# Kernel tuning notes

Measured on AMD Instinct MI355X. Metric: run time of the kernel, lower is better.

The kernel has to match this reference:

```python
import jax, jax.numpy as jnp
import numpy as np

N, E, W, G = 100000, 625000, 128, 64  # nodes, edges, width, num graphs
EPS = 1e-5


def setup_inputs() -> dict:
    key = jax.random.key(0)
    ks = jax.random.split(key, 8)
    x = jax.random.normal(ks[0], (N, W), jnp.float32)
    edge_index = jax.random.randint(ks[1], (2, E), 0, N, dtype=jnp.int32)
    edge_weight = jax.random.uniform(ks[2], (E,), jnp.float32)
    batch_map = jnp.sort(jax.random.randint(ks[3], (N,), 0, G, dtype=jnp.int32))
    s = 1.0 / np.sqrt(W)
    return {
        "x": x,
        "edge_index": edge_index,
        "edge_weight": edge_weight,
        "batch_map": batch_map,
        "gn_weight": jnp.ones((W,), jnp.float32),
        "gn_bias": jnp.zeros((W,), jnp.float32),
        "gn_mean_scale": jnp.ones((W,), jnp.float32),
        "W_rel1": jax.random.normal(ks[4], (W, W), jnp.float32) * s,
        "b_rel1": jnp.zeros((W,), jnp.float32),
        "W_root1": jax.random.normal(ks[5], (W, W), jnp.float32) * s,
        "W_rel2": jax.random.normal(ks[6], (W, W), jnp.float32) * s,
        "b_rel2": jnp.zeros((W,), jnp.float32),
        "W_root2": jax.random.normal(ks[7], (W, W), jnp.float32) * s,
    }


def _graph_norm(x, batch, weight, bias, mean_scale):
    # per-graph mean / var keyed on batch_map (PyG GraphNorm)
    cnt = jax.ops.segment_sum(jnp.ones((x.shape[0], 1), x.dtype), batch, num_segments=G)
    mean = jax.ops.segment_sum(x, batch, num_segments=G) / cnt
    out = x - mean_scale * mean[batch]
    var = jax.ops.segment_sum(out * out, batch, num_segments=G) / cnt
    std = jnp.sqrt(var + EPS)
    return weight * out / std[batch] + bias


def _graph_conv(x, src, dst, ew, W_rel, b_rel, W_root):
    # out_i = W_rel @ sum_{j->i} e_ji * x_j + b_rel + W_root @ x_i
    msg = x[src] * ew[:, None]                       # [E, W] gather
    agg = jax.ops.segment_sum(msg, dst, num_segments=x.shape[0])  # scatter-add
    return agg @ W_rel.T + b_rel + x @ W_root.T


def reference(x, edge_index, edge_weight, batch_map,
              gn_weight, gn_bias, gn_mean_scale,
              W_rel1, b_rel1, W_root1, W_rel2, b_rel2, W_root2):
    src, dst = edge_index[0], edge_index[1]
    xx = _graph_norm(x, batch_map, gn_weight, gn_bias, gn_mean_scale)
    xx = _graph_conv(xx, src, dst, edge_weight, W_rel1, b_rel1, W_root1)
    xx = jnp.where(xx >= 0, xx, 0.1 * xx)            # LeakyReLU(0.1)
    xx = _graph_conv(xx, src, dst, edge_weight, W_rel2, b_rel2, W_root2)
    return x + xx
```

## Files before the change

kernel.cpp:

```cpp
#include <hip/hip_runtime.h>
#include <hip/hip_bf16.h>

#define WW 128
#define GG 64
#define GN_EPS 1e-5f
#define SCAN_B 1024

typedef __attribute__((ext_vector_type(8))) short short8;
typedef __attribute__((ext_vector_type(4))) float floatx4;

__device__ inline float bf2f(__hip_bfloat16 h) { return __bfloat162float(h); }
__device__ inline float bfbits2f(short v) {
    return __uint_as_float(((unsigned)(unsigned short)v) << 16);
}
__device__ inline short f2bfbits(float f) {
    __hip_bfloat16 h = __float2bfloat16(f);
    return *reinterpret_cast<short*>(&h);
}

__global__ __launch_bounds__(128) void stats_kernel(
    const float* __restrict__ x, const int* __restrict__ batch, int N,
    float* __restrict__ gsum, float* __restrict__ gsumsq, float* __restrict__ gcnt)
{
    int w = threadIdx.x;
    int row0 = blockIdx.x * 64;
    int row1 = min(row0 + 64, N);
    float s = 0.f, ss = 0.f;
    int cur = batch[row0];
    int cnt = 0;
    auto flush = [&]() {
        atomicAdd(&gsum[cur * WW + w], s);
        atomicAdd(&gsumsq[cur * WW + w], ss);
        if (w == 0) atomicAdd(&gcnt[cur], (float)cnt);
        s = 0.f; ss = 0.f; cnt = 0;
    };
    int i = row0;
    for (; i + 4 <= row1; i += 4) {
        int g0 = batch[i + 0], g1 = batch[i + 1], g2 = batch[i + 2], g3 = batch[i + 3];
        float v0 = x[(size_t)(i + 0) * WW + w];
        float v1 = x[(size_t)(i + 1) * WW + w];
        float v2 = x[(size_t)(i + 2) * WW + w];
        float v3 = x[(size_t)(i + 3) * WW + w];
        if (g0 != cur) { flush(); cur = g0; }
        s += v0; ss += v0 * v0; ++cnt;
        if (g1 != cur) { flush(); cur = g1; }
        s += v1; ss += v1 * v1; ++cnt;
        if (g2 != cur) { flush(); cur = g2; }
        s += v2; ss += v2 * v2; ++cnt;
        if (g3 != cur) { flush(); cur = g3; }
        s += v3; ss += v3 * v3; ++cnt;
    }
    for (; i < row1; ++i) {
        int g = batch[i];
        float v = x[(size_t)i * WW + w];
        if (g != cur) { flush(); cur = g; }
        s += v; ss += v * v; ++cnt;
    }
    flush();
}

__global__ __launch_bounds__(256) void finalize_kernel(
    const float* __restrict__ gsum, const float* __restrict__ gsumsq,
    const float* __restrict__ gcnt,
    const float* __restrict__ wgt, const float* __restrict__ bias,
    const float* __restrict__ ms,
    float* __restrict__ scalev, float* __restrict__ shiftv)
{
    int idx = blockIdx.x * blockDim.x + threadIdx.x;
    if (idx >= GG * WW) return;
    int g = idx >> 7, w = idx & (WW - 1);
    float cnt = gcnt[g];
    float inv = cnt > 0.f ? 1.f / cnt : 0.f;
    float mean = gsum[idx] * inv;
    float msw = ms[w];
    float var = gsumsq[idx] * inv - mean * mean * msw * (2.f - msw);
    var = fmaxf(var, 0.f);
    float sc = wgt[w] * rsqrtf(var + GN_EPS);
    scalev[idx] = sc;
    shiftv[idx] = bias[w] - sc * msw * mean;
}

__global__ __launch_bounds__(256) void normalize_kernel(
    const float* __restrict__ x, const int* __restrict__ batch,
    const float* __restrict__ scalev, const float* __restrict__ shiftv,
    __hip_bfloat16* __restrict__ xn, int N)
{
    size_t tid = (size_t)blockIdx.x * blockDim.x + threadIdx.x;
    if (tid >= (size_t)N * (WW / 4)) return;
    int row = (int)(tid >> 5);
    int c4 = (int)(tid & 31) * 4;
    int g = batch[row];
    float4 v = *(const float4*)(x + (size_t)row * WW + c4);
    float4 sc = *(const float4*)(scalev + (size_t)g * WW + c4);
    float4 sh = *(const float4*)(shiftv + (size_t)g * WW + c4);
    __hip_bfloat162 o0, o1;
    o0.x = __float2bfloat16(sc.x * v.x + sh.x);
    o0.y = __float2bfloat16(sc.y * v.y + sh.y);
    o1.x = __float2bfloat16(sc.z * v.z + sh.z);
    o1.y = __float2bfloat16(sc.w * v.w + sh.w);
    union { __hip_bfloat162 h[2]; uint2 u; } pk;
    pk.h[0] = o0; pk.h[1] = o1;
    *(uint2*)(xn + (size_t)row * WW + c4) = pk.u;
}

__global__ __launch_bounds__(256) void cvt_w_kernel(
    const float* __restrict__ w0, const float* __restrict__ w1,
    const float* __restrict__ w2, const float* __restrict__ w3,
    __hip_bfloat16* __restrict__ dst)
{
    int idx = blockIdx.x * blockDim.x + threadIdx.x;
    int m = idx >> 14;
    int o = idx & 16383;
    const float* src = (m == 0) ? w0 : (m == 1) ? w1 : (m == 2) ? w2 : w3;
    dst[idx] = __float2bfloat16(src[o]);
}

__global__ __launch_bounds__(256) void hist_kernel(
    const int* __restrict__ ei, int E, int* __restrict__ deg)
{
    int e = blockIdx.x * 256 + threadIdx.x;
    if (e < E) atomicAdd(&deg[ei[(size_t)E + e]], 1);
}

__global__ __launch_bounds__(SCAN_B) void scan_blocks(
    const int* __restrict__ deg, int N, int* __restrict__ off, int* __restrict__ bsum)
{
    __shared__ int s[SCAN_B];
    int t = threadIdx.x;
    int i = blockIdx.x * SCAN_B + t;
    int v = (i < N) ? deg[i] : 0;
    s[t] = v; __syncthreads();
    for (int d = 1; d < SCAN_B; d <<= 1) {
        int tmp = (t >= d) ? s[t - d] : 0;
        __syncthreads();
        s[t] += tmp;
        __syncthreads();
    }
    if (i < N) off[i] = s[t] - v;
    if (t == SCAN_B - 1) bsum[blockIdx.x] = s[t];
}

__global__ __launch_bounds__(256) void scan_partials(int* __restrict__ bsum, int P)
{
    __shared__ int s[256];
    int t = threadIdx.x;
    int v = (t < P) ? bsum[t] : 0;
    s[t] = v; __syncthreads();
    for (int d = 1; d < 256; d <<= 1) {
        int tmp = (t >= d) ? s[t - d] : 0;
        __syncthreads();
        s[t] += tmp;
        __syncthreads();
    }
    if (t < P) bsum[t] = s[t] - v;
}

__global__ __launch_bounds__(SCAN_B) void add_offsets(
    int* __restrict__ off, const int* __restrict__ bsum, int N)
{
    int i = blockIdx.x * SCAN_B + threadIdx.x;
    if (i < N) off[i] += bsum[blockIdx.x];
}

__global__ __launch_bounds__(256) void place_kernel(
    const int* __restrict__ ei, const float* __restrict__ ew,
    const int* __restrict__ off, int* __restrict__ cursor,
    int2* __restrict__ ebuf, int E)
{
    int base = blockIdx.x * 1024 + threadIdx.x;
    int dstv[4], srcv[4];
    float wv[4];
    int slot[4];
#pragma unroll
    for (int i = 0; i < 4; ++i) {
        int e = base + i * 256;
        dstv[i] = (e < E) ? ei[(size_t)E + e] : -1;
    }
#pragma unroll
    for (int i = 0; i < 4; ++i) {
        int e = base + i * 256;
        if (e < E) { srcv[i] = ei[e]; wv[i] = ew[e]; }
    }
#pragma unroll
    for (int i = 0; i < 4; ++i)
        if (dstv[i] >= 0) slot[i] = off[dstv[i]] + atomicAdd(&cursor[dstv[i]], 1);
#pragma unroll
    for (int i = 0; i < 4; ++i)
        if (dstv[i] >= 0) ebuf[slot[i]] = make_int2(srcv[i], __float_as_int(wv[i]));
}

template <bool OUT_BF16>
__global__ __launch_bounds__(256, 4) void fused_kernel(
    const __hip_bfloat16* __restrict__ X,
    const int2* __restrict__ ebuf, const int* __restrict__ off,
    const int* __restrict__ deg,
    const __hip_bfloat16* __restrict__ Wrel, const __hip_bfloat16* __restrict__ Wroot,
    const float* __restrict__ bias, const float* __restrict__ resid,
    void* __restrict__ outv, int N, int leaky)
{
    __shared__ __hip_bfloat16 smem[2 * 32 * 128];
    int tid = threadIdx.x;
    int wave = tid >> 6, lane = tid & 63;
    int q = lane >> 4, r16 = lane & 15;
    int rb = blockIdx.x * 32;

#pragma unroll
    for (int s = 0; s < 2; ++s) {
        int t = wave * 2 + s;
        int rloc = t * 4 + (lane >> 4);
        int c = (lane & 15) ^ (rloc & 15);
        int grow = rb + rloc; if (grow >= N) grow = N - 1;
        const __hip_bfloat16* g = X + (size_t)grow * WW + c * 8;
        __hip_bfloat16* l = smem + 4096 + t * 512;
        __builtin_amdgcn_global_load_lds(
            (const __attribute__((address_space(1))) void*)g,
            (__attribute__((address_space(3))) void*)l, 16, 0, 0);
    }

    int node = rb + (tid >> 3);
    int nc = node < N ? node : N - 1;
    int start = off[nc];
    int d = (node < N) ? deg[nc] : 0;
    int sub = tid & 7;
    float a16[16];
#pragma unroll
    for (int j = 0; j < 16; ++j) a16[j] = 0.f;
    int last = start + d - 1;
    for (int k = start; k <= last; k += 2) {
        int i1 = min(k + 1, last);
        int2 p0 = ebuf[k];
        int2 p1 = ebuf[i1];
        const __hip_bfloat16* r0 = X + (size_t)p0.x * WW + sub * 16;
        const __hip_bfloat16* r1 = X + (size_t)p1.x * WW + sub * 16;
        short8 a0 = *(const short8*)(r0);
        short8 b0 = *(const short8*)(r0 + 8);
        short8 a1 = *(const short8*)(r1);
        short8 b1 = *(const short8*)(r1 + 8);
        float w0 = __int_as_float(p0.y);
        float w1 = (k + 1 <= last) ? __int_as_float(p1.y) : 0.f;
#pragma unroll
        for (int j = 0; j < 8; ++j) {
            a16[j]     += w0 * bfbits2f(a0[j]) + w1 * bfbits2f(a1[j]);
            a16[8 + j] += w0 * bfbits2f(b0[j]) + w1 * bfbits2f(b1[j]);
        }
    }

    {
        int r = tid >> 3;
        short8 pk0, pk1;
#pragma unroll
        for (int j = 0; j < 8; ++j) {
            pk0[j] = f2bfbits(a16[j]);
            pk1[j] = f2bfbits(a16[8 + j]);
        }
        int s0 = (2 * sub)     ^ (r & 15);
        int s1 = (2 * sub + 1) ^ (r & 15);
        *(short8*)(smem + r * 128 + s0 * 8) = pk0;
        *(short8*)(smem + r * 128 + s1 * 8) = pk1;
    }

    short8 wf[8][2];
#pragma unroll
    for (int kc = 0; kc < 8; ++kc) {
        const __hip_bfloat16* Wsel = (kc < 4) ? Wrel : Wroot;
        int koff = (kc & 3) * 32 + q * 8;
#pragma unroll
        for (int tt = 0; tt < 2; ++tt) {
            int col = wave * 32 + 2 * r16 + tt;
            wf[kc][tt] = *(const short8*)(Wsel + ((size_t)col * WW + koff));
        }
    }
    float bcol[2];
#pragma unroll
    for (int tt = 0; tt < 2; ++tt) bcol[tt] = bias[wave * 32 + 2 * r16 + tt];

    __syncthreads();

    floatx4 acc[2][2];
#pragma unroll
    for (int r = 0; r < 2; ++r)
#pragma unroll
        for (int tt = 0; tt < 2; ++tt) acc[r][tt] = (floatx4){0.f, 0.f, 0.f, 0.f};

#pragma unroll
    for (int kc = 0; kc < 8; ++kc) {
        int m = kc >> 2;
        short8 af[2];
#pragma unroll
        for (int r = 0; r < 2; ++r) {
            int row = r * 16 + r16;
            int slot = ((kc & 3) * 4 + q) ^ r16;
            af[r] = *(const short8*)(&smem[m * 4096 + row * 128 + slot * 8]);
        }
#pragma unroll
        for (int r = 0; r < 2; ++r) {
            acc[r][0] = __builtin_amdgcn_mfma_f32_16x16x32_bf16(af[r], wf[kc][0], acc[r][0], 0, 0, 0);
            acc[r][1] = __builtin_amdgcn_mfma_f32_16x16x32_bf16(af[r], wf[kc][1], acc[r][1], 0, 0, 0);
        }
    }

    int colb = wave * 32 + 2 * r16;
#pragma unroll
    for (int r = 0; r < 2; ++r)
#pragma unroll
        for (int rr = 0; rr < 4; ++rr) {
            int row = rb + r * 16 + q * 4 + rr;
            if (row < N) {
                float v0 = acc[r][0][rr] + bcol[0];
                float v1 = acc[r][1][rr] + bcol[1];
                if (leaky) {
                    v0 = v0 >= 0.f ? v0 : 0.1f * v0;
                    v1 = v1 >= 0.f ? v1 : 0.1f * v1;
                }
                if (OUT_BF16) {
                    __hip_bfloat162 o;
                    o.x = __float2bfloat16(v0);
                    o.y = __float2bfloat16(v1);
                    *(__hip_bfloat162*)((__hip_bfloat16*)outv + (size_t)row * WW + colb) = o;
                } else {
                    float2 rv = *(const float2*)(resid + (size_t)row * WW + colb);
                    float2 o;
                    o.x = v0 + rv.x;
                    o.y = v1 + rv.y;
                    *(float2*)((float*)outv + (size_t)row * WW + colb) = o;
                }
            }
        }
}

extern "C" void kernel_launch(void* const* d_in, const int* in_sizes, int n_in,
                              void* d_out, int out_size, void* d_ws, size_t ws_size,
                              hipStream_t stream) {
    const float* x      = (const float*)d_in[0];
    const int*   ei     = (const int*)d_in[1];
    const float* ew     = (const float*)d_in[2];
    const int*   batch  = (const int*)d_in[3];
    const float* gnw    = (const float*)d_in[4];
    const float* gnb    = (const float*)d_in[5];
    const float* gnm    = (const float*)d_in[6];
    const float* Wrel1  = (const float*)d_in[7];
    const float* brel1  = (const float*)d_in[8];
    const float* Wroot1 = (const float*)d_in[9];
    const float* Wrel2  = (const float*)d_in[10];
    const float* brel2  = (const float*)d_in[11];
    const float* Wroot2 = (const float*)d_in[12];

    int N = in_sizes[0] / WW;
    int E = in_sizes[1] / 2;
    int P = (N + SCAN_B - 1) / SCAN_B;
    int ntiles = (N + 31) / 32;

    __hip_bfloat16* xn = (__hip_bfloat16*)d_ws;
    __hip_bfloat16* y1 = xn + (size_t)N * WW;
    __hip_bfloat16* Wb = y1 + (size_t)N * WW;
    int2* ebuf   = (int2*)(Wb + 4 * WW * WW);
    int*  deg    = (int*)(ebuf + E);
    int*  cursor = deg + N;
    float* gsum   = (float*)(cursor + N);
    float* gsumsq = gsum + GG * WW;
    float* gcnt   = gsumsq + GG * WW;
    float* scalev = gcnt + GG;
    float* shiftv = scalev + GG * WW;
    int*  off    = (int*)(shiftv + GG * WW);
    int*  bsum   = off + N;

    hipMemsetAsync(deg, 0, ((size_t)2 * N + 2 * GG * WW + GG) * sizeof(int), stream);

    hist_kernel<<<(E + 255) / 256, 256, 0, stream>>>(ei, E, deg);
    scan_blocks<<<P, SCAN_B, 0, stream>>>(deg, N, off, bsum);
    scan_partials<<<1, 256, 0, stream>>>(bsum, P);
    add_offsets<<<P, SCAN_B, 0, stream>>>(off, bsum, N);
    place_kernel<<<(E + 1023) / 1024, 256, 0, stream>>>(ei, ew, off, cursor, ebuf, E);

    cvt_w_kernel<<<(4 * WW * WW) / 256, 256, 0, stream>>>(Wrel1, Wroot1, Wrel2, Wroot2, Wb);
    stats_kernel<<<(N + 63) / 64, 128, 0, stream>>>(x, batch, N, gsum, gsumsq, gcnt);
    finalize_kernel<<<(GG * WW + 255) / 256, 256, 0, stream>>>(
        gsum, gsumsq, gcnt, gnw, gnb, gnm, scalev, shiftv);
    normalize_kernel<<<(int)(((size_t)N * (WW / 4) + 255) / 256), 256, 0, stream>>>(
        x, batch, scalev, shiftv, xn, N);

    fused_kernel<true><<<ntiles, 256, 0, stream>>>(
        xn, ebuf, off, deg, Wb, Wb + WW * WW, brel1, nullptr, y1, N, 1);

    fused_kernel<false><<<ntiles, 256, 0, stream>>>(
        y1, ebuf, off, deg, Wb + 2 * WW * WW, Wb + 3 * WW * WW, brel2, x, d_out, N, 0);
}
```

Measured before the change: 327.5 us.

## Stage tile edge lists in LDS, unroll gather by four, halve stats rows per block

Each fused-kernel block now copies its 32-node contiguous CSR edge segment (up to 512 entries) into shared memory with async global-to-LDS loads, then reads edge pairs from LDS instead of global memory, falling back to global for overflow. The gather loop is unrolled from 2 to 4 edges per iteration to put more independent row loads in flight. The stats kernel processes 32 rows per block instead of 64 to raise parallelism, at the cost of more atomics. The staging adds a __syncthreads and extra LDS, which may lower occupancy.

```diff
diff --git a/kernel.cpp b/kernel.cpp
--- a/kernel.cpp
+++ b/kernel.cpp
@@ -23,8 +23,8 @@
     float* __restrict__ gsum, float* __restrict__ gsumsq, float* __restrict__ gcnt)
 {
     int w = threadIdx.x;
-    int row0 = blockIdx.x * 64;
-    int row1 = min(row0 + 64, N);
+    int row0 = blockIdx.x * 32;
+    int row1 = min(row0 + 32, N);
     float s = 0.f, ss = 0.f;
     int cur = batch[row0];
     int cnt = 0;
@@ -198,7 +198,8 @@
     const float* __restrict__ bias, const float* __restrict__ resid,
     void* __restrict__ outv, int N, int leaky)
 {
-    __shared__ __hip_bfloat16 smem[2 * 32 * 128];
+    __shared__ __align__(16) __hip_bfloat16 smem[2 * 32 * 128];
+    __shared__ __align__(16) int2 eshare[512];
     int tid = threadIdx.x;
     int wave = tid >> 6, lane = tid & 63;
     int q = lane >> 4, r16 = lane & 15;
@@ -217,31 +218,70 @@
             (__attribute__((address_space(3))) void*)l, 16, 0, 0);
     }
 
+    int endn = min(rb + 32, N) - 1;
+    int e0 = off[rb];
+    int ne = off[endn] + deg[endn] - e0;
+    int nstage = min(ne, 512);
+    {
+        int pairs = (nstage + 1) >> 1;
+        if (tid < pairs) {
+            const int2* g = ebuf + e0 + 2 * tid;
+            int2* l = eshare + 2 * (wave * 64);
+            __builtin_amdgcn_global_load_lds(
+                (const __attribute__((address_space(1))) void*)g,
+                (__attribute__((address_space(3))) void*)l, 16, 0, 0);
+        }
+    }
+    __syncthreads();
+
     int node = rb + (tid >> 3);
     int nc = node < N ? node : N - 1;
     int start = off[nc];
     int d = (node < N) ? deg[nc] : 0;
+    int lb = start - e0;
     int sub = tid & 7;
     float a16[16];
 #pragma unroll
     for (int j = 0; j < 16; ++j) a16[j] = 0.f;
-    int last = start + d - 1;
-    for (int k = start; k <= last; k += 2) {
-        int i1 = min(k + 1, last);
-        int2 p0 = ebuf[k];
-        int2 p1 = ebuf[i1];
+    int last = d - 1;
+    for (int k = 0; k <= last; k += 4) {
+        int j1 = min(k + 1, last);
+        int j2 = min(k + 2, last);
+        int j3 = min(k + 3, last);
+        int2 p0, p1, p2, p3;
+        if (lb + j3 < nstage) {
+            p0 = eshare[lb + k];
+            p1 = eshare[lb + j1];
+            p2 = eshare[lb + j2];
+            p3 = eshare[lb + j3];
+        } else {
+            p0 = (lb + k  < nstage) ? eshare[lb + k]  : ebuf[start + k];
+            p1 = (lb + j1 < nstage) ? eshare[lb + j1] : ebuf[start + j1];
+            p2 = (lb + j2 < nstage) ? eshare[lb + j2] : ebuf[start + j2];
+            p3 = (lb + j3 < nstage) ? eshare[lb + j3] : ebuf[start + j3];
+        }
         const __hip_bfloat16* r0 = X + (size_t)p0.x * WW + sub * 16;
         const __hip_bfloat16* r1 = X + (size_t)p1.x * WW + sub * 16;
+        const __hip_bfloat16* r2 = X + (size_t)p2.x * WW + sub * 16;
+        const __hip_bfloat16* r3 = X + (size_t)p3.x * WW + sub * 16;
         short8 a0 = *(const short8*)(r0);
         short8 b0 = *(const short8*)(r0 + 8);
         short8 a1 = *(const short8*)(r1);
         short8 b1 = *(const short8*)(r1 + 8);
+        short8 a2 = *(const short8*)(r2);
+        short8 b2 = *(const short8*)(r2 + 8);
+        short8 a3 = *(const short8*)(r3);
+        short8 b3 = *(const short8*)(r3 + 8);
         float w0 = __int_as_float(p0.y);
         float w1 = (k + 1 <= last) ? __int_as_float(p1.y) : 0.f;
+        float w2 = (k + 2 <= last) ? __int_as_float(p2.y) : 0.f;
+        float w3 = (k + 3 <= last) ? __int_as_float(p3.y) : 0.f;
 #pragma unroll
         for (int j = 0; j < 8; ++j) {
             a16[j]     += w0 * bfbits2f(a0[j]) + w1 * bfbits2f(a1[j]);
             a16[8 + j] += w0 * bfbits2f(b0[j]) + w1 * bfbits2f(b1[j]);
+            a16[j]     += w2 * bfbits2f(a2[j]) + w3 * bfbits2f(a3[j]);
+            a16[8 + j] += w2 * bfbits2f(b2[j]) + w3 * bfbits2f(b3[j]);
         }
     }
 
@@ -373,7 +413,7 @@
     place_kernel<<<(E + 1023) / 1024, 256, 0, stream>>>(ei, ew, off, cursor, ebuf, E);
 
     cvt_w_kernel<<<(4 * WW * WW) / 256, 256, 0, stream>>>(Wrel1, Wroot1, Wrel2, Wroot2, Wb);
-    stats_kernel<<<(N + 63) / 64, 128, 0, stream>>>(x, batch, N, gsum, gsumsq, gcnt);
+    stats_kernel<<<(N + 31) / 32, 128, 0, stream>>>(x, batch, N, gsum, gsumsq, gcnt);
     finalize_kernel<<<(GG * WW + 255) / 256, 256, 0, stream>>>(
         gsum, gsumsq, gcnt, gnw, gnb, gnm, scalev, shiftv);
     normalize_kernel<<<(int)(((size_t)N * (WW / 4) + 255) / 256), 256, 0, stream>>>(
```

Result: no change. 324.0 us (-1.1%).
